# Optimization experiments

Hardware: AMD Instinct MI355X
Metric: run time of the kernel (lower is better)

The kernel has to match this reference:

```python
import jax, jax.numpy as jnp
import numpy as np

NH, NKV, HD = 16, 4, 64   # n_heads, n_kv_heads, head_dim
N_REP = NH // NKV
EPS = 1e-6


def rms_norm(x, w):
    var = jnp.mean(x.astype(jnp.float32) ** 2, axis=-1, keepdims=True)
    return (x.astype(jnp.float32) * jax.lax.rsqrt(var + EPS)).astype(x.dtype) * w


def rotate_half(x):
    x1, x2 = jnp.split(x, 2, axis=-1)
    return jnp.concatenate([-x2, x1], axis=-1)


def setup_inputs() -> dict:
    key = jax.random.key(0)
    ks = jax.random.split(key, 6)
    B, S, H = 2, 2048, 2048
    x = jax.random.normal(ks[0], (B, S, H), dtype=jnp.float32)
    # RoPE tables [S, HD]
    inv_freq = 1.0 / (10000.0 ** (jnp.arange(0, HD, 2, dtype=jnp.float32) / HD))
    freqs = jnp.arange(S, dtype=jnp.float32)[:, None] * inv_freq[None, :]
    emb = jnp.concatenate([freqs, freqs], axis=-1)
    cos, sin = jnp.cos(emb), jnp.sin(emb)
    scale = 0.02
    wq = jax.random.normal(ks[1], (H, NH * HD), dtype=jnp.float32) * scale
    wk = jax.random.normal(ks[2], (H, NKV * HD), dtype=jnp.float32) * scale
    wv = jax.random.normal(ks[3], (H, NKV * HD), dtype=jnp.float32) * scale
    wo = jax.random.normal(ks[4], (NH * HD, H), dtype=jnp.float32) * scale
    q_norm_w = jnp.ones((HD,), dtype=jnp.float32)
    k_norm_w = jnp.ones((HD,), dtype=jnp.float32)
    return {"x": x, "cos": cos, "sin": sin, "wq": wq, "wk": wk, "wv": wv,
            "wo": wo, "q_norm_w": q_norm_w, "k_norm_w": k_norm_w}


def reference(x, cos, sin, wq, wk, wv, wo, q_norm_w, k_norm_w):
    B, S, H = x.shape
    # QKV projections + per-head RMSNorm on q/k
    q = rms_norm((x @ wq).reshape(B, S, NH, HD), q_norm_w)
    k = rms_norm((x @ wk).reshape(B, S, NKV, HD), k_norm_w)
    v = (x @ wv).reshape(B, S, NKV, HD)
    # RoPE (broadcast over heads)
    c = cos[None, :S, None, :]
    s = sin[None, :S, None, :]
    q = q * c + rotate_half(q) * s
    k = k * c + rotate_half(k) * s
    # prefill with S == window_size: no KV eviction, T == S -> causal mask
    k = jnp.repeat(k, N_REP, axis=2)  # [B,S,NH,HD]
    v = jnp.repeat(v, N_REP, axis=2)
    scores = jnp.einsum('bqhd,bkhd->bhqk', q, k) / jnp.sqrt(jnp.float32(HD))
    causal = jnp.triu(jnp.full((S, S), -jnp.inf, dtype=scores.dtype), 1)
    scores = scores + causal
    attn = jax.nn.softmax(scores.astype(jnp.float32), axis=-1).astype(q.dtype)
    out = jnp.einsum('bhqk,bkhd->bqhd', attn, v).reshape(B, S, NH * HD)
    return out @ wo
```

## Files before the change

kernel.cpp:

```cpp
#include <hip/hip_runtime.h>

typedef float floatx4 __attribute__((ext_vector_type(4)));
typedef __bf16 bfx8 __attribute__((ext_vector_type(8)));
typedef __bf16 bfx4 __attribute__((ext_vector_type(4)));

constexpr int B_ = 2, S_ = 2048, H_ = 2048, NH_ = 16, NKV_ = 4, HD_ = 64;
constexpr int M_ = B_ * S_;
constexpr int NQKV_ = NH_ * HD_ + 2 * NKV_ * HD_;
constexpr int HQ_ = NH_ * HD_;
constexpr int XP_ = 2056;
constexpr int AP_ = 1032;
constexpr int VP_ = 2056;

#define GLB(p) ((const __attribute__((address_space(1))) void*)(p))
#define LDS(p) ((__attribute__((address_space(3))) void*)(p))

__global__ __launch_bounds__(256) void cast_f32_bf16_pad(const float* __restrict__ src,
                                                         __bf16* __restrict__ dst) {
  int row = blockIdx.x;
  const float4* s = (const float4*)(src + (size_t)row * H_);
  __bf16* d = dst + (size_t)row * XP_;
#pragma unroll
  for (int i = 0; i < 2; i++) {
    int c = i * 256 + threadIdx.x;
    float4 v = s[c];
    bfx4 o;
    o[0] = (__bf16)v.x; o[1] = (__bf16)v.y; o[2] = (__bf16)v.z; o[3] = (__bf16)v.w;
    *(bfx4*)(d + c * 4) = o;
  }
}

__global__ __launch_bounds__(256) void transpose_cast(const float* __restrict__ src,
                                                      __bf16* __restrict__ dst,
                                                      int K, int N, int dstOff, int dstPitch) {
  __shared__ float tile[32][33];
  int n0 = blockIdx.x * 32, k0 = blockIdx.y * 32;
  int tx = threadIdx.x, ty = threadIdx.y;
#pragma unroll
  for (int r = 0; r < 32; r += 8)
    tile[ty + r][tx] = src[(size_t)(k0 + ty + r) * N + n0 + tx];
  __syncthreads();
#pragma unroll
  for (int r = 0; r < 32; r += 8)
    dst[(size_t)(n0 + ty + r + dstOff) * dstPitch + k0 + tx] = (__bf16)tile[tx][ty + r];
}

__global__ __launch_bounds__(256) void gemm_bf16_f32(const __bf16* __restrict__ A,
                                                     const __bf16* __restrict__ Bt,
                                                     float* __restrict__ C,
                                                     int M, int N, int K,
                                                     int lda, int ldb, int ldc) {
  __shared__ __align__(16) __bf16 As[128 * 64];
  __shared__ __align__(16) __bf16 Bs[128 * 64];
  int wid = threadIdx.x >> 6, lane = threadIdx.x & 63;
  int l15 = lane & 15, quad = lane >> 4;
  int wm = (wid >> 1) * 64, wn = (wid & 1) * 64;
  int m0 = blockIdx.y * 128, n0 = blockIdx.x * 128;
  int srow_off = lane >> 3;
  int gphys = lane & 7;
  floatx4 acc[4][4] = {};
  for (int kb = 0; kb < K; kb += 64) {
#pragma unroll
    for (int j = 0; j < 4; j++) {
      int rbase = wid * 32 + j * 8;
      int row = rbase + srow_off;
      int glog = gphys ^ (row & 7);
      const __bf16* ga = &A[(size_t)(m0 + row) * lda + kb + glog * 8];
      const __bf16* gb = &Bt[(size_t)(n0 + row) * ldb + kb + glog * 8];
      __builtin_amdgcn_global_load_lds(GLB(ga), LDS(&As[rbase * 64]), 16, 0, 0);
      __builtin_amdgcn_global_load_lds(GLB(gb), LDS(&Bs[rbase * 64]), 16, 0, 0);
    }
    __syncthreads();
#pragma unroll
    for (int kk = 0; kk < 64; kk += 32) {
      int cgq = (kk >> 3) + quad;
      bfx8 af[4], bfr[4];
#pragma unroll
      for (int mi = 0; mi < 4; mi++) {
        int row = wm + mi * 16 + l15;
        af[mi] = *(const bfx8*)&As[row * 64 + (cgq ^ (row & 7)) * 8];
      }
#pragma unroll
      for (int ni = 0; ni < 4; ni++) {
        int row = wn + ni * 16 + l15;
        bfr[ni] = *(const bfx8*)&Bs[row * 64 + (cgq ^ (row & 7)) * 8];
      }
#pragma unroll
      for (int mi = 0; mi < 4; mi++)
#pragma unroll
        for (int ni = 0; ni < 4; ni++)
          acc[mi][ni] = __builtin_amdgcn_mfma_f32_16x16x32_bf16(af[mi], bfr[ni], acc[mi][ni], 0, 0, 0);
    }
    __syncthreads();
  }
#pragma unroll
  for (int mi = 0; mi < 4; mi++)
#pragma unroll
    for (int ni = 0; ni < 4; ni++) {
      int row = m0 + wm + mi * 16 + quad * 4;
      int coln = n0 + wn + ni * 16 + l15;
#pragma unroll
      for (int r = 0; r < 4; r++)
        C[(size_t)(row + r) * ldc + coln] = acc[mi][ni][r];
    }
}

__global__ __launch_bounds__(256) void norm_rope_kernel(const float* __restrict__ qkv,
                                                        const float* __restrict__ cosT,
                                                        const float* __restrict__ sinT,
                                                        const float* __restrict__ qw,
                                                        const float* __restrict__ kw,
                                                        __bf16* __restrict__ Qo,
                                                        __bf16* __restrict__ Ko,
                                                        __bf16* __restrict__ VTo) {
  int s = blockIdx.x, b = blockIdx.y;
  int wid = threadIdx.x >> 6, lane = threadIdx.x & 63;
  const float* rowp = qkv + (size_t)(b * S_ + s) * NQKV_;
  float c = cosT[s * HD_ + lane];
  float sn = sinT[s * HD_ + lane];
#pragma unroll
  for (int it = 0; it < 5; it++) {
    int hh = it * 4 + wid;
    float v = rowp[hh * 64 + lane];
    float ss = v * v;
#pragma unroll
    for (int off = 1; off < 64; off <<= 1) ss += __shfl_xor(ss, off);
    float rs = rsqrtf(ss * (1.0f / 64.0f) + 1e-6f);
    const float* w = (hh < 16) ? qw : kw;
    float nv = v * rs * w[lane];
    float other = __shfl_xor(nv, 32);
    float rot = (lane < 32) ? -other : other;
    float outv = nv * c + rot * sn;
    if (hh < 16)
      Qo[(((size_t)b * NH_ + hh) * S_ + s) * HD_ + lane] = (__bf16)outv;
    else
      Ko[(((size_t)b * NKV_ + (hh - 16)) * S_ + s) * HD_ + lane] = (__bf16)outv;
  }
  {
    float v = rowp[(20 + wid) * 64 + lane];
    VTo[(((size_t)b * NKV_ + wid) * HD_ + lane) * VP_ + s] = (__bf16)v;
  }
}

__global__ __launch_bounds__(256, 4) void attn_kernel(const __bf16* __restrict__ Q,
                                                      const __bf16* __restrict__ Kc,
                                                      const __bf16* __restrict__ VT,
                                                      __bf16* __restrict__ Ob) {
  int px = blockIdx.x, h = blockIdx.y, b = blockIdx.z;
  int u = (px + 2 * (h & 7)) & 31;
  int qt = (((h >> 3) ^ b) & 1) ? (31 - u) : u;
  int wid = threadIdx.x >> 6, lane = threadIdx.x & 63;
  int l15 = lane & 15, quad = lane >> 4;
  int q0 = qt * 64 + wid * 16;
  int kvh = h >> 2;
  const __bf16* Qh = Q + (((size_t)b * NH_ + h) * S_ + q0) * HD_;
  const __bf16* Kh = Kc + ((size_t)b * NKV_ + kvh) * S_ * HD_;
  const __bf16* Vh = VT + ((size_t)b * NKV_ + kvh) * (size_t)HD_ * VP_;
  __shared__ __align__(16) __bf16 Ks[64][72];
  __shared__ __align__(16) __bf16 Vs[64][72];
  __shared__ __align__(16) __bf16 Pst[4][16][72];
  __bf16 (*P)[72] = Pst[wid];

  int srow = threadIdx.x >> 3;
  int scol = (threadIdx.x & 7) * 8;

  bfx8 qf0, qf1;
  {
    const __bf16* qp = Qh + l15 * HD_ + quad * 8;
    qf0 = *(const bfx8*)qp;
    qf1 = *(const bfx8*)(qp + 32);
  }
  floatx4 oacc[4] = {};
  float ps = 0.f;
  int ntiles = qt + 1;
  bfx8 kpre0, kpre1, vpre0, vpre1;
  kpre0 = *(const bfx8*)&Kh[(size_t)srow * HD_ + scol];
  kpre1 = *(const bfx8*)&Kh[(size_t)(srow + 32) * HD_ + scol];
  vpre0 = *(const bfx8*)&Vh[(size_t)srow * VP_ + scol];
  vpre1 = *(const bfx8*)&Vh[(size_t)(srow + 32) * VP_ + scol];
  for (int kt = 0; kt < ntiles; kt++) {
    int kv0 = kt * 64;
    int dq = q0 - kv0;
    __syncthreads();
    *(bfx8*)&Ks[srow][scol] = kpre0;
    *(bfx8*)&Ks[srow + 32][scol] = kpre1;
    *(bfx8*)&Vs[srow][scol] = vpre0;
    *(bfx8*)&Vs[srow + 32][scol] = vpre1;
    __syncthreads();
    if (kt + 1 < ntiles) {
      int kn = kv0 + 64;
      kpre0 = *(const bfx8*)&Kh[(size_t)(kn + srow) * HD_ + scol];
      kpre1 = *(const bfx8*)&Kh[(size_t)(kn + srow + 32) * HD_ + scol];
      vpre0 = *(const bfx8*)&Vh[(size_t)srow * VP_ + kn + scol];
      vpre1 = *(const bfx8*)&Vh[(size_t)(srow + 32) * VP_ + kn + scol];
    }
    floatx4 sf[4];
#pragma unroll
    for (int nt = 0; nt < 4; nt++) {
      bfx8 kf0 = *(const bfx8*)&Ks[nt * 16 + l15][quad * 8];
      bfx8 kf1 = *(const bfx8*)&Ks[nt * 16 + l15][32 + quad * 8];
      floatx4 z = {0.f, 0.f, 0.f, 0.f};
      z = __builtin_amdgcn_mfma_f32_16x16x32_bf16(kf0, qf0, z, 0, 0, 0);
      sf[nt] = __builtin_amdgcn_mfma_f32_16x16x32_bf16(kf1, qf1, z, 0, 0, 0);
    }
#pragma unroll
    for (int nt = 0; nt < 4; nt++) {
      bfx4 pk;
#pragma unroll
      for (int r = 0; r < 4; r++) {
        int kvrel = nt * 16 + quad * 4 + r;
        float p = __expf(sf[nt][r] * 0.125f);
        p = (kvrel - l15 > dq) ? 0.f : p;
        ps += p;
        pk[r] = (__bf16)p;
      }
      *(bfx4*)&P[l15][nt * 16 + quad * 4] = pk;
    }
    bfx8 pa0 = *(const bfx8*)&P[l15][quad * 8];
    bfx8 pa1 = *(const bfx8*)&P[l15][32 + quad * 8];
#pragma unroll
    for (int ot = 0; ot < 4; ot++) {
      bfx8 vf0 = *(const bfx8*)&Vs[ot * 16 + l15][quad * 8];
      bfx8 vf1 = *(const bfx8*)&Vs[ot * 16 + l15][32 + quad * 8];
      oacc[ot] = __builtin_amdgcn_mfma_f32_16x16x32_bf16(pa0, vf0, oacc[ot], 0, 0, 0);
      oacc[ot] = __builtin_amdgcn_mfma_f32_16x16x32_bf16(pa1, vf1, oacc[ot], 0, 0, 0);
    }
  }
  ps += __shfl_xor(ps, 16);
  ps += __shfl_xor(ps, 32);
  float rl[4];
#pragma unroll
  for (int r = 0; r < 4; r++) rl[r] = 1.0f / __shfl(ps, quad * 4 + r);
#pragma unroll
  for (int ot = 0; ot < 4; ot++)
#pragma unroll
    for (int r = 0; r < 4; r++) {
      float val = oacc[ot][r] * rl[r];
      Ob[((size_t)b * S_ + q0 + quad * 4 + r) * AP_ + h * HD_ + ot * 16 + l15] = (__bf16)val;
    }
}

extern "C" void kernel_launch(void* const* d_in, const int* in_sizes, int n_in,
                              void* d_out, int out_size, void* d_ws, size_t ws_size,
                              hipStream_t stream) {
  const float* x   = (const float*)d_in[0];
  const float* cosT = (const float*)d_in[1];
  const float* sinT = (const float*)d_in[2];
  const float* wq  = (const float*)d_in[3];
  const float* wk  = (const float*)d_in[4];
  const float* wv  = (const float*)d_in[5];
  const float* wo  = (const float*)d_in[6];
  const float* qw  = (const float*)d_in[7];
  const float* kw  = (const float*)d_in[8];
  float* out = (float*)d_out;

  char* w = (char*)d_ws;
  __bf16* xbf   = (__bf16*)(w);
  __bf16* wqkvT = (__bf16*)(w + 16842752);
  __bf16* woT   = (__bf16*)(w + 23158784);
  float*  qkv   = (float*) (w + 27385856);
  __bf16* attnO = (__bf16*)(w + 27385856);
  __bf16* Qb    = (__bf16*)(w + 52551680);
  __bf16* Kb    = (__bf16*)(w + 60940288);
  __bf16* VTb   = (__bf16*)(w + 63037440);

  cast_f32_bf16_pad<<<M_, 256, 0, stream>>>(x, xbf);
  dim3 tb(32, 8);
  transpose_cast<<<dim3(1024 / 32, 2048 / 32), tb, 0, stream>>>(wq, wqkvT, 2048, 1024, 0,    XP_);
  transpose_cast<<<dim3(256 / 32, 2048 / 32),  tb, 0, stream>>>(wk, wqkvT, 2048, 256,  1024, XP_);
  transpose_cast<<<dim3(256 / 32, 2048 / 32),  tb, 0, stream>>>(wv, wqkvT, 2048, 256,  1280, XP_);
  transpose_cast<<<dim3(2048 / 32, 1024 / 32), tb, 0, stream>>>(wo, woT,   1024, 2048, 0,    AP_);
  gemm_bf16_f32<<<dim3(NQKV_ / 128, M_ / 128), 256, 0, stream>>>(xbf, wqkvT, qkv, M_, NQKV_, H_, XP_, XP_, NQKV_);
  norm_rope_kernel<<<dim3(S_, B_), 256, 0, stream>>>(qkv, cosT, sinT, qw, kw, Qb, Kb, VTb);
  attn_kernel<<<dim3(32, NH_, B_), 256, 0, stream>>>(Qb, Kb, VTb, attnO);
  gemm_bf16_f32<<<dim3(H_ / 128, M_ / 128), 256, 0, stream>>>(attnO, woT, out, M_, H_, HQ_, AP_, AP_, H_);
}
```

Baseline: 244.4 us.

## Split-K the QKV GEMM and fuse input cast/transpose kernels into one launch

Merges the x cast and the four weight transpose-cast launches into a single prep kernel that dispatches on block index. The QKV projection GEMM is run as split-K with two halves writing separate fp32 partial buffers, and norm_rope sums the partials when it reads them. The goal is better CU occupancy on the QKV GEMM, whose grid was otherwise about 1.5 waves, and fewer launch overheads. The cost is extra workspace and extra fp32 traffic for the second partial buffer.

```diff
diff --git a/kernel.cpp b/kernel.cpp
--- a/kernel.cpp
+++ b/kernel.cpp
@@ -11,55 +11,69 @@
 constexpr int XP_ = 2056;
 constexpr int AP_ = 1032;
 constexpr int VP_ = 2056;
+constexpr int QKV_ELEMS_ = M_ * NQKV_;
 
 #define GLB(p) ((const __attribute__((address_space(1))) void*)(p))
 #define LDS(p) ((__attribute__((address_space(3))) void*)(p))
 
-__global__ __launch_bounds__(256) void cast_f32_bf16_pad(const float* __restrict__ src,
-                                                         __bf16* __restrict__ dst) {
-  int row = blockIdx.x;
-  const float4* s = (const float4*)(src + (size_t)row * H_);
-  __bf16* d = dst + (size_t)row * XP_;
-#pragma unroll
-  for (int i = 0; i < 2; i++) {
-    int c = i * 256 + threadIdx.x;
-    float4 v = s[c];
-    bfx4 o;
-    o[0] = (__bf16)v.x; o[1] = (__bf16)v.y; o[2] = (__bf16)v.z; o[3] = (__bf16)v.w;
-    *(bfx4*)(d + c * 4) = o;
-  }
-}
-
-__global__ __launch_bounds__(256) void transpose_cast(const float* __restrict__ src,
-                                                      __bf16* __restrict__ dst,
-                                                      int K, int N, int dstOff, int dstPitch) {
+__global__ __launch_bounds__(256) void prep_kernel(const float* __restrict__ x,
+                                                   const float* __restrict__ wq,
+                                                   const float* __restrict__ wk,
+                                                   const float* __restrict__ wv,
+                                                   const float* __restrict__ wo,
+                                                   __bf16* __restrict__ xbf,
+                                                   __bf16* __restrict__ wqkvT,
+                                                   __bf16* __restrict__ woT) {
   __shared__ float tile[32][33];
-  int n0 = blockIdx.x * 32, k0 = blockIdx.y * 32;
-  int tx = threadIdx.x, ty = threadIdx.y;
+  int bid = blockIdx.x;
+  if (bid < M_) {
+    const float4* s = (const float4*)(x + (size_t)bid * H_);
+    __bf16* d = xbf + (size_t)bid * XP_;
+#pragma unroll
+    for (int i = 0; i < 2; i++) {
+      int c = i * 256 + threadIdx.x;
+      float4 v = s[c];
+      bfx4 o;
+      o[0] = (__bf16)v.x; o[1] = (__bf16)v.y; o[2] = (__bf16)v.z; o[3] = (__bf16)v.w;
+      *(bfx4*)(d + c * 4) = o;
+    }
+    return;
+  }
+  bid -= M_;
+  const float* src; __bf16* dst; int N, dstOff, pitch, nbx;
+  if (bid < 2048)      { src = wq; dst = wqkvT; N = 1024; dstOff = 0;    pitch = XP_; nbx = 32; }
+  else if (bid < 2560) { bid -= 2048; src = wk; dst = wqkvT; N = 256; dstOff = 1024; pitch = XP_; nbx = 8; }
+  else if (bid < 3072) { bid -= 2560; src = wv; dst = wqkvT; N = 256; dstOff = 1280; pitch = XP_; nbx = 8; }
+  else                 { bid -= 3072; src = wo; dst = woT;   N = 2048; dstOff = 0;   pitch = AP_; nbx = 64; }
+  int n0 = (bid % nbx) * 32, k0 = (bid / nbx) * 32;
+  int tx = threadIdx.x & 31, ty = threadIdx.x >> 5;
 #pragma unroll
   for (int r = 0; r < 32; r += 8)
     tile[ty + r][tx] = src[(size_t)(k0 + ty + r) * N + n0 + tx];
   __syncthreads();
 #pragma unroll
   for (int r = 0; r < 32; r += 8)
-    dst[(size_t)(n0 + ty + r + dstOff) * dstPitch + k0 + tx] = (__bf16)tile[tx][ty + r];
+    dst[(size_t)(n0 + ty + r + dstOff) * pitch + k0 + tx] = (__bf16)tile[tx][ty + r];
 }
 
 __global__ __launch_bounds__(256) void gemm_bf16_f32(const __bf16* __restrict__ A,
                                                      const __bf16* __restrict__ Bt,
                                                      float* __restrict__ C,
                                                      int M, int N, int K,
-                                                     int lda, int ldb, int ldc) {
+                                                     int lda, int ldb, int ldc,
+                                                     unsigned long long cstride) {
   __shared__ __align__(16) __bf16 As[128 * 64];
   __shared__ __align__(16) __bf16 Bs[128 * 64];
   int wid = threadIdx.x >> 6, lane = threadIdx.x & 63;
   int l15 = lane & 15, quad = lane >> 4;
   int wm = (wid >> 1) * 64, wn = (wid & 1) * 64;
   int m0 = blockIdx.y * 128, n0 = blockIdx.x * 128;
+  int kb0 = blockIdx.z * K;
+  C += (size_t)blockIdx.z * cstride;
   int srow_off = lane >> 3;
   int gphys = lane & 7;
   floatx4 acc[4][4] = {};
-  for (int kb = 0; kb < K; kb += 64) {
+  for (int kb = kb0; kb < kb0 + K; kb += 64) {
 #pragma unroll
     for (int j = 0; j < 4; j++) {
       int rbase = wid * 32 + j * 8;
@@ -116,12 +130,14 @@
   int s = blockIdx.x, b = blockIdx.y;
   int wid = threadIdx.x >> 6, lane = threadIdx.x & 63;
   const float* rowp = qkv + (size_t)(b * S_ + s) * NQKV_;
+  const float* rowp2 = rowp + QKV_ELEMS_;
   float c = cosT[s * HD_ + lane];
   float sn = sinT[s * HD_ + lane];
 #pragma unroll
   for (int it = 0; it < 5; it++) {
     int hh = it * 4 + wid;
-    float v = rowp[hh * 64 + lane];
+    int idx = hh * 64 + lane;
+    float v = rowp[idx] + rowp2[idx];
     float ss = v * v;
 #pragma unroll
     for (int off = 1; off < 64; off <<= 1) ss += __shfl_xor(ss, off);
@@ -137,7 +153,8 @@
       Ko[(((size_t)b * NKV_ + (hh - 16)) * S_ + s) * HD_ + lane] = (__bf16)outv;
   }
   {
-    float v = rowp[(20 + wid) * 64 + lane];
+    int idx = (20 + wid) * 64 + lane;
+    float v = rowp[idx] + rowp2[idx];
     VTo[(((size_t)b * NKV_ + wid) * HD_ + lane) * VP_ + s] = (__bf16)v;
   }
 }
@@ -260,18 +277,15 @@
   __bf16* woT   = (__bf16*)(w + 23158784);
   float*  qkv   = (float*) (w + 27385856);
   __bf16* attnO = (__bf16*)(w + 27385856);
-  __bf16* Qb    = (__bf16*)(w + 52551680);
-  __bf16* Kb    = (__bf16*)(w + 60940288);
-  __bf16* VTb   = (__bf16*)(w + 63037440);
-
-  cast_f32_bf16_pad<<<M_, 256, 0, stream>>>(x, xbf);
-  dim3 tb(32, 8);
-  transpose_cast<<<dim3(1024 / 32, 2048 / 32), tb, 0, stream>>>(wq, wqkvT, 2048, 1024, 0,    XP_);
-  transpose_cast<<<dim3(256 / 32, 2048 / 32),  tb, 0, stream>>>(wk, wqkvT, 2048, 256,  1024, XP_);
-  transpose_cast<<<dim3(256 / 32, 2048 / 32),  tb, 0, stream>>>(wv, wqkvT, 2048, 256,  1280, XP_);
-  transpose_cast<<<dim3(2048 / 32, 1024 / 32), tb, 0, stream>>>(wo, woT,   1024, 2048, 0,    AP_);
-  gemm_bf16_f32<<<dim3(NQKV_ / 128, M_ / 128), 256, 0, stream>>>(xbf, wqkvT, qkv, M_, NQKV_, H_, XP_, XP_, NQKV_);
+  __bf16* Qb    = (__bf16*)(w + 77717504);
+  __bf16* Kb    = (__bf16*)(w + 86106112);
+  __bf16* VTb   = (__bf16*)(w + 88203264);
+
+  prep_kernel<<<M_ + 5120, 256, 0, stream>>>(x, wq, wk, wv, wo, xbf, wqkvT, woT);
+  gemm_bf16_f32<<<dim3(NQKV_ / 128, M_ / 128, 2), 256, 0, stream>>>(
+      xbf, wqkvT, qkv, M_, NQKV_, H_ / 2, XP_, XP_, NQKV_, (unsigned long long)QKV_ELEMS_);
   norm_rope_kernel<<<dim3(S_, B_), 256, 0, stream>>>(qkv, cosT, sinT, qw, kw, Qb, Kb, VTb);
   attn_kernel<<<dim3(32, NH_, B_), 256, 0, stream>>>(Qb, Kb, VTb, attnO);
-  gemm_bf16_f32<<<dim3(H_ / 128, M_ / 128), 256, 0, stream>>>(attnO, woT, out, M_, H_, HQ_, AP_, AP_, H_);
-}
+  gemm_bf16_f32<<<dim3(H_ / 128, M_ / 128, 1), 256, 0, stream>>>(
+      attnO, woT, out, M_, H_, HQ_, AP_, AP_, H_, 0ull);
+}
```

After: 240.8 us. Within noise of the previous version (-1.5%).
